# Kernel tuning notes

Measured on AMD Instinct MI355X. Metric: run time of the kernel, lower is better.

Reference implementation:

```python
import jax, jax.numpy as jnp
import numpy as np

DIM = 512
HEADS = 4
DH = 128          # dim_head
CHUNK = 16        # chunk_size
MAX_LR = 0.01     # default_adaptive_step_transform max_lr
EPS = 1e-6        # flax RMSNorm epsilon


def setup_inputs() -> dict:
    key = jax.random.key(0)
    ks = jax.random.split(key, 8)
    B, S = 2, 2048
    dim_inner = HEADS * DH
    seq = jax.random.normal(ks[0], (B, S, DIM), jnp.float32)
    store_norm_scale = jnp.ones((DIM,), jnp.float32)               # RMSNorm scale
    W_kv = (jax.random.normal(ks[1], (DIM, 2 * dim_inner)) * 0.02).astype(jnp.float32)
    W_step = (jax.random.normal(ks[2], (DIM, HEADS)) * 0.02).astype(jnp.float32)
    W_mom = (jax.random.normal(ks[3], (DIM, HEADS)) * 0.02).astype(jnp.float32)
    W_decay = (jax.random.normal(ks[4], (DIM, HEADS)) * 0.02).astype(jnp.float32)
    # past memory-MLP weights, shared init expanded to (b, h, dh, dh)
    w0 = jnp.broadcast_to((jax.random.normal(ks[5], (DH, DH)) * 0.02).astype(jnp.float32), (B, HEADS, DH, DH)) + 0.0
    w1 = jnp.broadcast_to((jax.random.normal(ks[6], (DH, DH)) * 0.02).astype(jnp.float32), (B, HEADS, DH, DH)) + 0.0
    return {"seq": seq, "store_norm_scale": store_norm_scale, "W_kv": W_kv,
            "W_step": W_step, "W_mom": W_mom, "W_decay": W_decay, "w0": w0, "w1": w1}


def _mlp(w0, w1, x):
    # MemoryMLP depth=2: x @ w0 ; silu ; @ w1
    return jax.nn.silu(x @ w0) @ w1


def _chunk_loss(w0, w1, k, lr, v):
    pred = _mlp(w0, w1, k)                       # [c, d]
    return jnp.sum(jnp.mean((pred - v) ** 2, axis=-1) * lr)


def _binop(e1, e2):
    a1, b1 = e1
    a2, b2 = e2
    return a1 * a2, a2 * b1 + b2


def _lin_scan(a, b):
    # first-order linear recurrence y_t = a_t * y_{t-1} + b_t along chunk axis (axis=2)
    return jax.lax.associative_scan(_binop, (a, b), axis=2)[1]


def _store(seq, store_norm_scale, W_kv, W_step, W_mom, W_decay, w0, w1):
    B, S, _ = seq.shape
    n = S // CHUNK
    # pre RMSNorm (with scale)
    x = seq * jax.lax.rsqrt(jnp.mean(seq * seq, axis=-1, keepdims=True) + EPS) * store_norm_scale
    # adaptive per-token lr:  sigmoid(x @ W_step) * max_lr  -> [b, h, s]
    lr = jax.nn.sigmoid(jnp.einsum('bsd,dh->bhs', x, W_step)) * MAX_LR
    # per-chunk mean -> momentum / decay factors  [b, h, n, 1]
    mean = x.reshape(B, n, CHUNK, DIM).mean(axis=2)
    mom = jax.nn.sigmoid(jnp.einsum('bnd,dh->bhn', mean, W_mom))[..., None]
    dec = jax.nn.sigmoid(jnp.einsum('bnd,dh->bhn', mean, W_decay))[..., None]
    # keys / values  [b*h, n, c, dh]
    kv = x @ W_kv
    k, v = jnp.split(kv, 2, axis=-1)
    k = k.reshape(B, n, CHUNK, HEADS, DH).transpose(0, 3, 1, 2, 4).reshape(B * HEADS, n, CHUNK, DH)
    v = v.reshape(B, n, CHUNK, HEADS, DH).transpose(0, 3, 1, 2, 4).reshape(B * HEADS, n, CHUNK, DH)
    lr_ch = lr.reshape(B, HEADS, n, CHUNK).reshape(B * HEADS, n, CHUNK)
    w0bh = w0.reshape(B * HEADS, DH, DH)
    w1bh = w1.reshape(B * HEADS, DH, DH)
    # per-chunk gradients of the MLP loss at the *past* weights (all chunks independent)
    gfn = jax.grad(_chunk_loss, argnums=(0, 1))
    gfn = jax.vmap(gfn, in_axes=(None, None, 0, 0, 0))   # over chunks n
    gfn = jax.vmap(gfn, in_axes=(0, 0, 0, 0, 0))         # over b*h
    g0, g1 = gfn(w0bh, w1bh, k, lr_ch, v)                # [b*h, n, dh, dh]
    s0 = (-g0).reshape(B, HEADS, n, DH * DH)             # surprises
    s1 = (-g1).reshape(B, HEADS, n, DH * DH)
    # momentum scan then decay scan (Titans update rule)
    m0 = _lin_scan(jnp.broadcast_to(mom, s0.shape), s0)
    m1 = _lin_scan(jnp.broadcast_to(mom, s1.shape), s1)
    u0 = _lin_scan(jnp.broadcast_to(1.0 - dec, m0.shape), m0)
    u1 = _lin_scan(jnp.broadcast_to(1.0 - dec, m1.shape), m1)
    updates = jnp.stack([u0.reshape(B, HEADS, n, DH, DH),
                         u1.reshape(B, HEADS, n, DH, DH)], axis=0)  # [2, b, h, n, dh, dh]
    return updates


def reference(seq, store_norm_scale, W_kv, W_step, W_mom, W_decay, w0, w1):
    return _store(seq, store_norm_scale, W_kv, W_step, W_mom, W_decay, w0, w1)
```

## Files before the change

kernel.cpp:

```cpp
#include <hip/hip_runtime.h>

#define DIMX 512
#define HEADSX 4
#define DHX 128
#define CHX 16
#define NCX 128
#define SX 2048
#define BX 2
#define BHX 8
#define PADF 136

typedef unsigned short ushort_t;
typedef unsigned int uint_t;
typedef short bf16x8 __attribute__((ext_vector_type(8)));
typedef float f32x4 __attribute__((ext_vector_type(4)));

__device__ __forceinline__ float sigmoidf_(float z){ return 1.0f/(1.0f + __expf(-z)); }

__device__ __forceinline__ ushort_t f2bf(float f){
  uint_t u = __float_as_uint(f);
  return (ushort_t)((u + 0x7FFFu + ((u >> 16) & 1u)) >> 16);
}
__device__ __forceinline__ uint_t pk2(float a, float b){
  return (uint_t)f2bf(a) | ((uint_t)f2bf(b) << 16);
}

__global__ __launch_bounds__(256) void k_prep(const float* __restrict__ Wkv,
    const float* __restrict__ w0, const float* __restrict__ w1,
    const float* __restrict__ scale,
    const float* __restrict__ Wstep, const float* __restrict__ Wmom,
    const float* __restrict__ Wdec,
    ushort_t* __restrict__ WkvT, ushort_t* __restrict__ w0T,
    ushort_t* __restrict__ w1T, ushort_t* __restrict__ w1n,
    float* __restrict__ wfsS, float* __restrict__ wfsM, float* __restrict__ wfsD){
  int blk = blockIdx.x; int tid = threadIdx.x;
  if (blk < 64){
    int h = blk >> 4, kt = blk & 15;
    __shared__ ushort_t tile[256][33];
    for (int i=tid; i<8192; i+=256){
      int kk = i >> 8, col = i & 255;
      int d = kt*32 + kk;
      int wcol = (col < 128) ? (h*128 + col) : (384 + h*128 + col);
      float v = scale[d] * Wkv[(size_t)d*1024 + wcol];
      tile[col][kk] = f2bf(v);
    }
    __syncthreads();
    for (int i=tid; i<8192; i+=256){
      int col = i >> 5, kk = i & 31;
      WkvT[(((size_t)h*16 + kt)*256 + col)*32 + kk] = tile[col][kk];
    }
  } else if (blk < 72){
    int bh = blk - 64;
    size_t base = (size_t)bh*16384;
    for (int i=tid; i<16384; i+=256){
      int r = i >> 7, c = i & 127;
      w0T[base + i] = f2bf(w0[base + (size_t)c*128 + r]);
      w1T[base + i] = f2bf(w1[base + (size_t)c*128 + r]);
      w1n[base + i] = f2bf(w1[base + i]);
    }
  } else {
    for (int i=tid; i<2048; i+=256){
      int d = i & 511, h = i >> 9;
      float sc = scale[d];
      wfsS[i] = sc * Wstep[d*4 + h];
      wfsM[i] = sc * Wmom [d*4 + h];
      wfsD[i] = sc * Wdec [d*4 + h];
    }
  }
}

__global__ __launch_bounds__(256) void k_fused3(const float* __restrict__ seq,
    const float* __restrict__ wfsS, const float* __restrict__ wfsM,
    const float* __restrict__ wfsD,
    const ushort_t* __restrict__ WkvT, const ushort_t* __restrict__ w0T,
    const ushort_t* __restrict__ w1T, const ushort_t* __restrict__ w1n,
    ushort_t* __restrict__ fac0, ushort_t* __restrict__ fac1,
    float* __restrict__ momw, float* __restrict__ decw){
  int blk = blockIdx.x;
  int bh = blk & 7, tq = blk >> 3;
  int b = bh >> 2, h = bh & 3;
  int tid = threadIdx.x;
  int wv = tid >> 6, lane = tid & 63;
  int t = tq*4 + wv;
  int bt = bh*NCX + t;
  int quad = lane >> 4, nl = lane & 15;
  const f32x4 zero = {0.f,0.f,0.f,0.f};

  __shared__ __align__(16) ushort_t ks_[4][16*PADF];
  __shared__ __align__(16) ushort_t as_[4][16*PADF];
  __shared__ __align__(16) ushort_t dp_[4][16*PADF];
  __shared__ __align__(16) ushort_t dh_[4][16*PADF];
  __shared__ float lr_s[4][16];
  ushort_t* ksw = ks_[wv]; ushort_t* asw = as_[wv];
  ushort_t* dpw = dp_[wv]; ushort_t* dhw = dh_[wv];

  const float* sq = seq + ((size_t)(b*SX + t*CHX) + nl)*DIMX + quad*8;
  const float* wS = wfsS + h*512 + quad*8;
  const float* wM = wfsM + h*512 + quad*8;
  const float* wD = wfsD + h*512 + quad*8;

  float ss=0.f, lp=0.f, pm=0.f, pd=0.f;
  #pragma unroll
  for (int kt=0; kt<16; kt++){
    float4 q0 = *(const float4*)(sq + kt*32);
    float4 q1 = *(const float4*)(sq + kt*32 + 4);
    float4 s0 = *(const float4*)(wS + kt*32);
    float4 s1 = *(const float4*)(wS + kt*32 + 4);
    float4 m0 = *(const float4*)(wM + kt*32);
    float4 m1 = *(const float4*)(wM + kt*32 + 4);
    float4 d0 = *(const float4*)(wD + kt*32);
    float4 d1 = *(const float4*)(wD + kt*32 + 4);
    ss += q0.x*q0.x + q0.y*q0.y + q0.z*q0.z + q0.w*q0.w
        + q1.x*q1.x + q1.y*q1.y + q1.z*q1.z + q1.w*q1.w;
    lp += q0.x*s0.x + q0.y*s0.y + q0.z*s0.z + q0.w*s0.w
        + q1.x*s1.x + q1.y*s1.y + q1.z*s1.z + q1.w*s1.w;
    pm += q0.x*m0.x + q0.y*m0.y + q0.z*m0.z + q0.w*m0.w
        + q1.x*m1.x + q1.y*m1.y + q1.z*m1.z + q1.w*m1.w;
    pd += q0.x*d0.x + q0.y*d0.y + q0.z*d0.z + q0.w*d0.w
        + q1.x*d1.x + q1.y*d1.y + q1.z*d1.z + q1.w*d1.w;
  }
  #pragma unroll
  for (int mk=16; mk<64; mk<<=1){
    ss += __shfl_xor(ss, mk, 64); lp += __shfl_xor(lp, mk, 64);
    pm += __shfl_xor(pm, mk, 64); pd += __shfl_xor(pd, mk, 64);
  }
  float rs = 1.0f / sqrtf(ss*(1.0f/DIMX) + 1e-6f);
  float lr = 0.01f * sigmoidf_(rs*lp);
  float pmr = rs*pm, pdr = rs*pd;
  #pragma unroll
  for (int mk=1; mk<16; mk<<=1){
    pmr += __shfl_xor(pmr, mk, 64); pdr += __shfl_xor(pdr, mk, 64);
  }
  if (lane==0){
    momw[bt] = sigmoidf_(pmr*(1.0f/CHX));
    decw[bt] = 1.0f - sigmoidf_(pdr*(1.0f/CHX));
  }
  if (quad==0) lr_s[wv][nl] = lr;

  union BF { bf16x8 v; uint_t u[4]; };
  f32x4 kacc[8], vacc[8];
  #pragma unroll
  for (int s=0;s<8;s++){ kacc[s]=zero; vacc[s]=zero; }
  const ushort_t* wkvh = WkvT + (size_t)h*16*256*32;
  for (int kt=0; kt<16; kt++){
    float4 q0 = *(const float4*)(sq + kt*32);
    float4 q1 = *(const float4*)(sq + kt*32 + 4);
    BF af;
    af.u[0] = pk2(q0.x*rs, q0.y*rs);
    af.u[1] = pk2(q0.z*rs, q0.w*rs);
    af.u[2] = pk2(q1.x*rs, q1.y*rs);
    af.u[3] = pk2(q1.z*rs, q1.w*rs);
    const ushort_t* wb = wkvh + ((size_t)kt*256 + nl)*32 + quad*8;
    #pragma unroll
    for (int s=0; s<8; s++){
      bf16x8 Bk = *(const bf16x8*)(wb + (size_t)(s*16)*32);
      kacc[s] = __builtin_amdgcn_mfma_f32_16x16x32_bf16(af.v, Bk, kacc[s], 0,0,0);
      bf16x8 Bv = *(const bf16x8*)(wb + (size_t)(128 + s*16)*32);
      vacc[s] = __builtin_amdgcn_mfma_f32_16x16x32_bf16(af.v, Bv, vacc[s], 0,0,0);
    }
  }
  #pragma unroll
  for (int s=0;s<8;s++){
    #pragma unroll
    for (int r=0;r<4;r++)
      ksw[(quad*4+r)*PADF + s*16 + nl] = f2bf(kacc[s][r]);
  }

  const ushort_t* w0b = w0T + (size_t)bh*16384;
  f32x4 hacc[8];
  #pragma unroll
  for (int s=0;s<8;s++) hacc[s]=zero;
  for (int kt=0; kt<4; kt++){
    bf16x8 Af = *(const bf16x8*)&ksw[nl*PADF + kt*32 + quad*8];
    #pragma unroll
    for (int s=0; s<8; s++){
      bf16x8 Bf = *(const bf16x8*)&w0b[(size_t)(s*16+nl)*128 + kt*32 + quad*8];
      hacc[s] = __builtin_amdgcn_mfma_f32_16x16x32_bf16(Af, Bf, hacc[s], 0,0,0);
    }
  }
  float sp[8][4];
  #pragma unroll
  for (int s=0;s<8;s++){
    #pragma unroll
    for (int r=0;r<4;r++){
      float hh = hacc[s][r];
      float sg = sigmoidf_(hh);
      float a  = hh*sg;
      sp[s][r] = sg*(1.0f + hh*(1.0f-sg));
      asw[(quad*4+r)*PADF + s*16 + nl] = f2bf(a);
    }
  }

  const ushort_t* w1tb = w1T + (size_t)bh*16384;
  f32x4 pacc[8];
  #pragma unroll
  for (int s=0;s<8;s++) pacc[s]=zero;
  for (int kt=0; kt<4; kt++){
    bf16x8 Af = *(const bf16x8*)&asw[nl*PADF + kt*32 + quad*8];
    #pragma unroll
    for (int s=0; s<8; s++){
      bf16x8 Bf = *(const bf16x8*)&w1tb[(size_t)(s*16+nl)*128 + kt*32 + quad*8];
      pacc[s] = __builtin_amdgcn_mfma_f32_16x16x32_bf16(Af, Bf, pacc[s], 0,0,0);
    }
  }
  float lrv[4];
  #pragma unroll
  for (int r=0;r<4;r++) lrv[r] = lr_s[wv][quad*4 + r];
  #pragma unroll
  for (int s=0;s<8;s++){
    #pragma unroll
    for (int r=0;r<4;r++){
      float dp = (2.0f/DHX)*lrv[r]*(pacc[s][r] - vacc[s][r]);
      dpw[(quad*4+r)*PADF + s*16 + nl] = f2bf(dp);
    }
  }

  const ushort_t* w1nb = w1n + (size_t)bh*16384;
  f32x4 dacc[8];
  #pragma unroll
  for (int s=0;s<8;s++) dacc[s]=zero;
  for (int kt=0; kt<4; kt++){
    bf16x8 Af = *(const bf16x8*)&dpw[nl*PADF + kt*32 + quad*8];
    #pragma unroll
    for (int s=0; s<8; s++){
      bf16x8 Bf = *(const bf16x8*)&w1nb[(size_t)(s*16+nl)*128 + kt*32 + quad*8];
      dacc[s] = __builtin_amdgcn_mfma_f32_16x16x32_bf16(Af, Bf, dacc[s], 0,0,0);
    }
  }
  #pragma unroll
  for (int s=0;s<8;s++){
    #pragma unroll
    for (int r=0;r<4;r++)
      dhw[(quad*4+r)*PADF + s*16 + nl] = f2bf(dacc[s][r]*sp[s][r]);
  }

  #pragma unroll
  for (int j=0;j<2;j++){
    int p = lane + j*64;
    ushort_t rowv[32];
    #pragma unroll
    for (int c=0;c<16;c++){ rowv[c] = ksw[c*PADF + p]; rowv[16+c] = asw[c*PADF + p]; }
    {
      ushort_t* dst = fac0 + ((size_t)bt*128 + p)*32;
      const uint4* rv = (const uint4*)rowv;
      uint4* dq = (uint4*)dst;
      dq[0]=rv[0]; dq[1]=rv[1]; dq[2]=rv[2]; dq[3]=rv[3];
    }
    #pragma unroll
    for (int c=0;c<16;c++){ rowv[c] = dhw[c*PADF + p]; rowv[16+c] = dpw[c*PADF + p]; }
    {
      ushort_t* dst = fac1 + ((size_t)bt*128 + p)*32;
      const uint4* rv = (const uint4*)rowv;
      uint4* dq = (uint4*)dst;
      dq[0]=rv[0]; dq[1]=rv[1]; dq[2]=rv[2]; dq[3]=rv[3];
    }
  }
}

__global__ __launch_bounds__(64) void k_scan3(const ushort_t* __restrict__ fac0,
    const ushort_t* __restrict__ fac1,
    const float* __restrict__ momw, const float* __restrict__ decw,
    float* __restrict__ out){
  int blk = blockIdx.x;
  int bh  = blk & 7;
  int jb  = (blk >> 3) & 7;
  int ig  = (blk >> 6) & 7;
  int mat = blk >> 9;
  int lane = threadIdx.x;
  int quad = lane >> 4, rrow = lane & 15;
  const f32x4 zero = {0.f,0.f,0.f,0.f};
  const bf16x8 fz = {0,0,0,0,0,0,0,0};

  size_t rowbase = (size_t)bh*NCX*128;
  const ushort_t* pa = fac0 + (rowbase + (size_t)(ig*16 + rrow))*32 + mat*16 + quad*8;
  const ushort_t* pb = fac1 + (rowbase + (size_t)(jb*16 + rrow))*32 + mat*16 + quad*8;
  bool act = (quad < 2);

  bf16x8 fa0=fz, fb0=fz, fa1=fz, fb1=fz;
  if (act){
    fa0 = *(const bf16x8*)(pa);
    fb0 = *(const bf16x8*)(pb);
    fa1 = *(const bf16x8*)(pa + 4096);
    fb1 = *(const bf16x8*)(pb + 4096);
  }

  f32x4 m_ = zero, u_ = zero;
  size_t obase = ((size_t)(mat*BHX + bh)*NCX)*((size_t)DHX*DHX)
               + (size_t)(ig*16 + quad*4)*DHX + (size_t)(jb*16 + rrow);
  const float* mop = momw + bh*NCX;
  const float* dep = decw + bh*NCX;

  for (int t=0; t<NCX; t+=2){
    bf16x8 na0=fz, nb0=fz, na1=fz, nb1=fz;
    if (act && (t+2 < NCX)){
      na0 = *(const bf16x8*)(pa + (size_t)(t+2)*4096);
      nb0 = *(const bf16x8*)(pb + (size_t)(t+2)*4096);
      na1 = *(const bf16x8*)(pa + (size_t)(t+3)*4096);
      nb1 = *(const bf16x8*)(pb + (size_t)(t+3)*4096);
    }
    float mo = mop[t], de = dep[t];
    f32x4 g = __builtin_amdgcn_mfma_f32_16x16x32_bf16(fa0, fb0, zero, 0,0,0);
    float* ob = out + obase + (size_t)t*(DHX*DHX);
    #pragma unroll
    for (int r=0;r<4;r++){
      m_[r] = mo*m_[r] - g[r];
      u_[r] = de*u_[r] + m_[r];
      ob[(size_t)r*DHX] = u_[r];
    }
    mo = mop[t+1]; de = dep[t+1];
    g = __builtin_amdgcn_mfma_f32_16x16x32_bf16(fa1, fb1, zero, 0,0,0);
    ob += (size_t)DHX*DHX;
    #pragma unroll
    for (int r=0;r<4;r++){
      m_[r] = mo*m_[r] - g[r];
      u_[r] = de*u_[r] + m_[r];
      ob[(size_t)r*DHX] = u_[r];
    }
    fa0=na0; fb0=nb0; fa1=na1; fb1=nb1;
  }
}

extern "C" void kernel_launch(void* const* d_in, const int* in_sizes, int n_in,
                              void* d_out, int out_size, void* d_ws, size_t ws_size,
                              hipStream_t stream) {
  (void)in_sizes; (void)n_in; (void)out_size; (void)ws_size;
  const float* seq   = (const float*)d_in[0];
  const float* scale = (const float*)d_in[1];
  const float* Wkv   = (const float*)d_in[2];
  const float* Wstep = (const float*)d_in[3];
  const float* Wmom  = (const float*)d_in[4];
  const float* Wdec  = (const float*)d_in[5];
  const float* w0    = (const float*)d_in[6];
  const float* w1    = (const float*)d_in[7];
  float* out = (float*)d_out;

  ushort_t* fac0 = (ushort_t*)d_ws;
  ushort_t* fac1 = fac0 + 4194304;
  ushort_t* WkvT = fac1 + 4194304;
  ushort_t* w0T  = WkvT + 524288;
  ushort_t* w1T  = w0T + 131072;
  ushort_t* w1n  = w1T + 131072;
  float*    momw = (float*)(w1n + 131072);
  float*    decw = momw + 1024;
  float*    wfsS = decw + 1024;
  float*    wfsM = wfsS + 2048;
  float*    wfsD = wfsM + 2048;

  k_prep<<<dim3(73), dim3(256), 0, stream>>>(Wkv, w0, w1, scale, Wstep, Wmom, Wdec,
      WkvT, w0T, w1T, w1n, wfsS, wfsM, wfsD);
  k_fused3<<<dim3(256), dim3(256), 0, stream>>>(seq, wfsS, wfsM, wfsD,
      WkvT, w0T, w1T, w1n, fac0, fac1, momw, decw);
  k_scan3<<<dim3(1024), dim3(64), 0, stream>>>(fac0, fac1, momw, decw, out);
}
```

Before: 244.0 us.

## Split fused kernel into stats, KV GEMM and per-chunk MLP kernels

Replaces the single fused kernel with three stages. A stats kernel computes the RMSNorm, lr, momentum and decay per token once and writes a bf16 normalized input. A KV GEMM kernel computes keys and values once for all heads. A per-chunk MLP-gradient kernel then runs with more blocks and the MLP output columns spread across waves. The old fused kernel re-read seq four times per head and held large accumulator arrays per wave, which limited occupancy. The new layout adds global round-trips for xhat, k and v (v kept in fp32) plus two extra launches.

```diff
diff --git a/kernel.cpp b/kernel.cpp
--- a/kernel.cpp
+++ b/kernel.cpp
@@ -25,30 +25,36 @@
   return (uint_t)f2bf(a) | ((uint_t)f2bf(b) << 16);
 }
 
-__global__ __launch_bounds__(256) void k_prep(const float* __restrict__ Wkv,
+__global__ __launch_bounds__(256) void k_prep2(const float* __restrict__ Wkv,
     const float* __restrict__ w0, const float* __restrict__ w1,
     const float* __restrict__ scale,
     const float* __restrict__ Wstep, const float* __restrict__ Wmom,
     const float* __restrict__ Wdec,
-    ushort_t* __restrict__ WkvT, ushort_t* __restrict__ w0T,
+    ushort_t* __restrict__ WkvT2, ushort_t* __restrict__ w0T,
     ushort_t* __restrict__ w1T, ushort_t* __restrict__ w1n,
     float* __restrict__ wfsS, float* __restrict__ wfsM, float* __restrict__ wfsD){
   int blk = blockIdx.x; int tid = threadIdx.x;
   if (blk < 64){
-    int h = blk >> 4, kt = blk & 15;
-    __shared__ ushort_t tile[256][33];
-    for (int i=tid; i<8192; i+=256){
-      int kk = i >> 8, col = i & 255;
-      int d = kt*32 + kk;
-      int wcol = (col < 128) ? (h*128 + col) : (384 + h*128 + col);
-      float v = scale[d] * Wkv[(size_t)d*1024 + wcol];
-      tile[col][kk] = f2bf(v);
+    int n0 = blk*16;
+    __shared__ ushort_t tile[16][520];
+    #pragma unroll
+    for (int rr=0; rr<2; rr++){
+      int k = tid*2 + rr;
+      float sc = scale[k];
+      #pragma unroll
+      for (int f=0; f<4; f++){
+        float4 v = *(const float4*)&Wkv[(size_t)k*1024 + n0 + f*4];
+        tile[f*4+0][k] = f2bf(sc*v.x);
+        tile[f*4+1][k] = f2bf(sc*v.y);
+        tile[f*4+2][k] = f2bf(sc*v.z);
+        tile[f*4+3][k] = f2bf(sc*v.w);
+      }
     }
     __syncthreads();
-    for (int i=tid; i<8192; i+=256){
-      int col = i >> 5, kk = i & 31;
-      WkvT[(((size_t)h*16 + kt)*256 + col)*32 + kk] = tile[col][kk];
-    }
+    int nr = tid >> 4, seg = tid & 15;
+    const uint4* s = (const uint4*)&tile[nr][seg*32];
+    uint4* d = (uint4*)&WkvT2[(size_t)(n0+nr)*512 + seg*32];
+    d[0]=s[0]; d[1]=s[1]; d[2]=s[2]; d[3]=s[3];
   } else if (blk < 72){
     int bh = blk - 64;
     size_t base = (size_t)bh*16384;
@@ -60,198 +66,248 @@
     }
   } else {
     for (int i=tid; i<2048; i+=256){
-      int d = i & 511, h = i >> 9;
-      float sc = scale[d];
-      wfsS[i] = sc * Wstep[d*4 + h];
-      wfsM[i] = sc * Wmom [d*4 + h];
-      wfsD[i] = sc * Wdec [d*4 + h];
-    }
-  }
-}
-
-__global__ __launch_bounds__(256) void k_fused3(const float* __restrict__ seq,
+      float sc = scale[i>>2];
+      wfsS[i] = sc * Wstep[i];
+      wfsM[i] = sc * Wmom [i];
+      wfsD[i] = sc * Wdec [i];
+    }
+  }
+}
+
+__global__ __launch_bounds__(256) void k_stats2(const float* __restrict__ seq,
     const float* __restrict__ wfsS, const float* __restrict__ wfsM,
     const float* __restrict__ wfsD,
-    const ushort_t* __restrict__ WkvT, const ushort_t* __restrict__ w0T,
-    const ushort_t* __restrict__ w1T, const ushort_t* __restrict__ w1n,
-    ushort_t* __restrict__ fac0, ushort_t* __restrict__ fac1,
+    ushort_t* __restrict__ xhat, float* __restrict__ lrbuf,
     float* __restrict__ momw, float* __restrict__ decw){
   int blk = blockIdx.x;
-  int bh = blk & 7, tq = blk >> 3;
-  int b = bh >> 2, h = bh & 3;
+  int b = blk >> 7, nc = blk & 127;
   int tid = threadIdx.x;
   int wv = tid >> 6, lane = tid & 63;
-  int t = tq*4 + wv;
-  int bt = bh*NCX + t;
+  int c = tid >> 4, sl = tid & 15;
+  size_t tok = (size_t)(b*SX + nc*CHX + c);
+  const float4* sr = (const float4*)(seq + tok*DIMX);
+  float4 q[8];
+  #pragma unroll
+  for (int jj=0; jj<8; jj++) q[jj] = sr[sl + 16*jj];
+
+  float ss=0.f;
+  float lp[4]={0,0,0,0}, pm[4]={0,0,0,0}, pd[4]={0,0,0,0};
+  #pragma unroll
+  for (int jj=0; jj<8; jj++){
+    int d0 = (sl + 16*jj)*4;
+    float qx=q[jj].x, qy=q[jj].y, qz=q[jj].z, qw=q[jj].w;
+    ss += qx*qx + qy*qy + qz*qz + qw*qw;
+    #pragma unroll
+    for (int e=0; e<4; e++){
+      float qe = (e==0)?qx:(e==1)?qy:(e==2)?qz:qw;
+      float4 tS = *(const float4*)&wfsS[(size_t)(d0+e)*4];
+      float4 tM = *(const float4*)&wfsM[(size_t)(d0+e)*4];
+      float4 tD = *(const float4*)&wfsD[(size_t)(d0+e)*4];
+      lp[0]+=qe*tS.x; lp[1]+=qe*tS.y; lp[2]+=qe*tS.z; lp[3]+=qe*tS.w;
+      pm[0]+=qe*tM.x; pm[1]+=qe*tM.y; pm[2]+=qe*tM.z; pm[3]+=qe*tM.w;
+      pd[0]+=qe*tD.x; pd[1]+=qe*tD.y; pd[2]+=qe*tD.z; pd[3]+=qe*tD.w;
+    }
+  }
+  #pragma unroll
+  for (int mk=1; mk<16; mk<<=1){
+    ss += __shfl_xor(ss, mk, 64);
+    #pragma unroll
+    for (int hh=0; hh<4; hh++){
+      lp[hh]+=__shfl_xor(lp[hh],mk,64);
+      pm[hh]+=__shfl_xor(pm[hh],mk,64);
+      pd[hh]+=__shfl_xor(pd[hh],mk,64);
+    }
+  }
+  float rs = 1.0f / sqrtf(ss*(1.0f/DIMX) + 1e-6f);
+
+  #pragma unroll
+  for (int jj=0; jj<8; jj++){
+    uint2 u;
+    u.x = pk2(q[jj].x*rs, q[jj].y*rs);
+    u.y = pk2(q[jj].z*rs, q[jj].w*rs);
+    *(uint2*)&xhat[tok*DIMX + (size_t)(sl+16*jj)*4] = u;
+  }
+  if (sl == 0){
+    #pragma unroll
+    for (int hh=0; hh<4; hh++)
+      lrbuf[(size_t)(b*HEADSX+hh)*SX + nc*CHX + c] = 0.01f * sigmoidf_(rs*lp[hh]);
+  }
+  float pmr[4], pdr[4];
+  #pragma unroll
+  for (int hh=0; hh<4; hh++){ pmr[hh]=rs*pm[hh]; pdr[hh]=rs*pd[hh]; }
+  #pragma unroll
+  for (int mk=16; mk<64; mk<<=1){
+    #pragma unroll
+    for (int hh=0; hh<4; hh++){
+      pmr[hh]+=__shfl_xor(pmr[hh],mk,64);
+      pdr[hh]+=__shfl_xor(pdr[hh],mk,64);
+    }
+  }
+  __shared__ float redm[4][4], redd[4][4];
+  if (lane == 0){
+    #pragma unroll
+    for (int hh=0; hh<4; hh++){ redm[wv][hh]=pmr[hh]; redd[wv][hh]=pdr[hh]; }
+  }
+  __syncthreads();
+  if (tid < 8){
+    int hh = tid & 3; bool isd = tid >= 4;
+    float v = isd ? (redd[0][hh]+redd[1][hh]+redd[2][hh]+redd[3][hh])
+                  : (redm[0][hh]+redm[1][hh]+redm[2][hh]+redm[3][hh]);
+    float sg = sigmoidf_(v*(1.0f/CHX));
+    int bt = (b*HEADSX+hh)*NCX + nc;
+    if (isd) decw[bt] = 1.0f - sg; else momw[bt] = sg;
+  }
+}
+
+__global__ __launch_bounds__(512) void k_kv2(const ushort_t* __restrict__ xhat,
+    const ushort_t* __restrict__ WkvT2,
+    ushort_t* __restrict__ kbuf, float* __restrict__ vbuf){
+  int blk = blockIdx.x;
+  int nb = blk >> 6, mb = blk & 63;
+  int b = mb >> 5;
+  int mrow0 = (mb & 31) * 64;
+  int isv = nb >> 2, h = nb & 3;
+  int bh = b*HEADSX + h;
+  int tid = threadIdx.x;
+  int wv = tid >> 6, lane = tid & 63;
   int quad = lane >> 4, nl = lane & 15;
   const f32x4 zero = {0.f,0.f,0.f,0.f};
 
-  __shared__ __align__(16) ushort_t ks_[4][16*PADF];
-  __shared__ __align__(16) ushort_t as_[4][16*PADF];
-  __shared__ __align__(16) ushort_t dp_[4][16*PADF];
-  __shared__ __align__(16) ushort_t dh_[4][16*PADF];
-  __shared__ float lr_s[4][16];
-  ushort_t* ksw = ks_[wv]; ushort_t* asw = as_[wv];
-  ushort_t* dpw = dp_[wv]; ushort_t* dhw = dh_[wv];
-
-  const float* sq = seq + ((size_t)(b*SX + t*CHX) + nl)*DIMX + quad*8;
-  const float* wS = wfsS + h*512 + quad*8;
-  const float* wM = wfsM + h*512 + quad*8;
-  const float* wD = wfsD + h*512 + quad*8;
-
-  float ss=0.f, lp=0.f, pm=0.f, pd=0.f;
+  const ushort_t* xb = xhat + ((size_t)b*SX + mrow0)*DIMX + nl*DIMX + quad*8;
+  const ushort_t* brow = WkvT2 + ((size_t)nb*128 + wv*16 + nl)*DIMX + quad*8;
+
+  f32x4 acc[4] = {zero,zero,zero,zero};
   #pragma unroll
   for (int kt=0; kt<16; kt++){
-    float4 q0 = *(const float4*)(sq + kt*32);
-    float4 q1 = *(const float4*)(sq + kt*32 + 4);
-    float4 s0 = *(const float4*)(wS + kt*32);
-    float4 s1 = *(const float4*)(wS + kt*32 + 4);
-    float4 m0 = *(const float4*)(wM + kt*32);
-    float4 m1 = *(const float4*)(wM + kt*32 + 4);
-    float4 d0 = *(const float4*)(wD + kt*32);
-    float4 d1 = *(const float4*)(wD + kt*32 + 4);
-    ss += q0.x*q0.x + q0.y*q0.y + q0.z*q0.z + q0.w*q0.w
-        + q1.x*q1.x + q1.y*q1.y + q1.z*q1.z + q1.w*q1.w;
-    lp += q0.x*s0.x + q0.y*s0.y + q0.z*s0.z + q0.w*s0.w
-        + q1.x*s1.x + q1.y*s1.y + q1.z*s1.z + q1.w*s1.w;
-    pm += q0.x*m0.x + q0.y*m0.y + q0.z*m0.z + q0.w*m0.w
-        + q1.x*m1.x + q1.y*m1.y + q1.z*m1.z + q1.w*m1.w;
-    pd += q0.x*d0.x + q0.y*d0.y + q0.z*d0.z + q0.w*d0.w
-        + q1.x*d1.x + q1.y*d1.y + q1.z*d1.z + q1.w*d1.w;
-  }
-  #pragma unroll
-  for (int mk=16; mk<64; mk<<=1){
-    ss += __shfl_xor(ss, mk, 64); lp += __shfl_xor(lp, mk, 64);
-    pm += __shfl_xor(pm, mk, 64); pd += __shfl_xor(pd, mk, 64);
-  }
-  float rs = 1.0f / sqrtf(ss*(1.0f/DIMX) + 1e-6f);
-  float lr = 0.01f * sigmoidf_(rs*lp);
-  float pmr = rs*pm, pdr = rs*pd;
-  #pragma unroll
-  for (int mk=1; mk<16; mk<<=1){
-    pmr += __shfl_xor(pmr, mk, 64); pdr += __shfl_xor(pdr, mk, 64);
-  }
-  if (lane==0){
-    momw[bt] = sigmoidf_(pmr*(1.0f/CHX));
-    decw[bt] = 1.0f - sigmoidf_(pdr*(1.0f/CHX));
-  }
-  if (quad==0) lr_s[wv][nl] = lr;
-
-  union BF { bf16x8 v; uint_t u[4]; };
-  f32x4 kacc[8], vacc[8];
-  #pragma unroll
-  for (int s=0;s<8;s++){ kacc[s]=zero; vacc[s]=zero; }
-  const ushort_t* wkvh = WkvT + (size_t)h*16*256*32;
-  for (int kt=0; kt<16; kt++){
-    float4 q0 = *(const float4*)(sq + kt*32);
-    float4 q1 = *(const float4*)(sq + kt*32 + 4);
-    BF af;
-    af.u[0] = pk2(q0.x*rs, q0.y*rs);
-    af.u[1] = pk2(q0.z*rs, q0.w*rs);
-    af.u[2] = pk2(q1.x*rs, q1.y*rs);
-    af.u[3] = pk2(q1.z*rs, q1.w*rs);
-    const ushort_t* wb = wkvh + ((size_t)kt*256 + nl)*32 + quad*8;
-    #pragma unroll
-    for (int s=0; s<8; s++){
-      bf16x8 Bk = *(const bf16x8*)(wb + (size_t)(s*16)*32);
-      kacc[s] = __builtin_amdgcn_mfma_f32_16x16x32_bf16(af.v, Bk, kacc[s], 0,0,0);
-      bf16x8 Bv = *(const bf16x8*)(wb + (size_t)(128 + s*16)*32);
-      vacc[s] = __builtin_amdgcn_mfma_f32_16x16x32_bf16(af.v, Bv, vacc[s], 0,0,0);
-    }
-  }
-  #pragma unroll
-  for (int s=0;s<8;s++){
-    #pragma unroll
-    for (int r=0;r<4;r++)
-      ksw[(quad*4+r)*PADF + s*16 + nl] = f2bf(kacc[s][r]);
-  }
+    bf16x8 Bf = *(const bf16x8*)(brow + kt*32);
+    #pragma unroll
+    for (int mf=0; mf<4; mf++){
+      bf16x8 Af = *(const bf16x8*)(xb + (size_t)(mf*16)*DIMX + kt*32);
+      acc[mf] = __builtin_amdgcn_mfma_f32_16x16x32_bf16(Af, Bf, acc[mf], 0,0,0);
+    }
+  }
+  int p = wv*16 + nl;
+  #pragma unroll
+  for (int mf=0; mf<4; mf++){
+    int t = (mb & 31)*4 + mf;
+    size_t bt = (size_t)bh*NCX + t;
+    if (isv){
+      #pragma unroll
+      for (int r=0;r<4;r++)
+        vbuf[(bt*16 + quad*4 + r)*128 + p] = acc[mf][r];
+    } else {
+      #pragma unroll
+      for (int r=0;r<4;r++)
+        kbuf[(bt*16 + quad*4 + r)*128 + p] = f2bf(acc[mf][r]);
+    }
+  }
+}
+
+__global__ __launch_bounds__(128) void k_mlp2(const ushort_t* __restrict__ kbuf,
+    const float* __restrict__ vbuf, const float* __restrict__ lrbuf,
+    const ushort_t* __restrict__ w0T, const ushort_t* __restrict__ w1T,
+    const ushort_t* __restrict__ w1n,
+    ushort_t* __restrict__ fac0, ushort_t* __restrict__ fac1){
+  int blk = blockIdx.x;
+  int bh = blk & 7, t = blk >> 3;
+  size_t bt = (size_t)bh*NCX + t;
+  int tid = threadIdx.x;
+  int wv = tid >> 6, lane = tid & 63;
+  int quad = lane >> 4, nl = lane & 15;
+  const f32x4 zero = {0.f,0.f,0.f,0.f};
+  __shared__ __align__(16) ushort_t as_[16*PADF];
+  __shared__ __align__(16) ushort_t dp_[16*PADF];
+  __shared__ __align__(16) ushort_t dh_[16*PADF];
+
+  const ushort_t* kb = kbuf + bt*16*128;
 
   const ushort_t* w0b = w0T + (size_t)bh*16384;
-  f32x4 hacc[8];
-  #pragma unroll
-  for (int s=0;s<8;s++) hacc[s]=zero;
+  f32x4 hacc[4] = {zero,zero,zero,zero};
+  #pragma unroll
   for (int kt=0; kt<4; kt++){
-    bf16x8 Af = *(const bf16x8*)&ksw[nl*PADF + kt*32 + quad*8];
-    #pragma unroll
-    for (int s=0; s<8; s++){
-      bf16x8 Bf = *(const bf16x8*)&w0b[(size_t)(s*16+nl)*128 + kt*32 + quad*8];
-      hacc[s] = __builtin_amdgcn_mfma_f32_16x16x32_bf16(Af, Bf, hacc[s], 0,0,0);
-    }
-  }
-  float sp[8][4];
-  #pragma unroll
-  for (int s=0;s<8;s++){
-    #pragma unroll
-    for (int r=0;r<4;r++){
-      float hh = hacc[s][r];
+    bf16x8 Af = *(const bf16x8*)(kb + (size_t)nl*128 + kt*32 + quad*8);
+    #pragma unroll
+    for (int j=0; j<4; j++){
+      int n = (wv*4+j)*16 + nl;
+      bf16x8 Bf = *(const bf16x8*)(w0b + (size_t)n*128 + kt*32 + quad*8);
+      hacc[j] = __builtin_amdgcn_mfma_f32_16x16x32_bf16(Af, Bf, hacc[j], 0,0,0);
+    }
+  }
+  float sp[4][4];
+  #pragma unroll
+  for (int j=0; j<4; j++){
+    #pragma unroll
+    for (int r=0; r<4; r++){
+      float hh = hacc[j][r];
       float sg = sigmoidf_(hh);
-      float a  = hh*sg;
-      sp[s][r] = sg*(1.0f + hh*(1.0f-sg));
-      asw[(quad*4+r)*PADF + s*16 + nl] = f2bf(a);
-    }
-  }
+      sp[j][r] = sg*(1.0f + hh*(1.0f-sg));
+      as_[(quad*4+r)*PADF + (wv*4+j)*16 + nl] = f2bf(hh*sg);
+    }
+  }
+  __syncthreads();
 
   const ushort_t* w1tb = w1T + (size_t)bh*16384;
-  f32x4 pacc[8];
-  #pragma unroll
-  for (int s=0;s<8;s++) pacc[s]=zero;
+  f32x4 pacc[4] = {zero,zero,zero,zero};
+  #pragma unroll
   for (int kt=0; kt<4; kt++){
-    bf16x8 Af = *(const bf16x8*)&asw[nl*PADF + kt*32 + quad*8];
-    #pragma unroll
-    for (int s=0; s<8; s++){
-      bf16x8 Bf = *(const bf16x8*)&w1tb[(size_t)(s*16+nl)*128 + kt*32 + quad*8];
-      pacc[s] = __builtin_amdgcn_mfma_f32_16x16x32_bf16(Af, Bf, pacc[s], 0,0,0);
+    bf16x8 Af = *(const bf16x8*)&as_[nl*PADF + kt*32 + quad*8];
+    #pragma unroll
+    for (int j=0; j<4; j++){
+      int n = (wv*4+j)*16 + nl;
+      bf16x8 Bf = *(const bf16x8*)(w1tb + (size_t)n*128 + kt*32 + quad*8);
+      pacc[j] = __builtin_amdgcn_mfma_f32_16x16x32_bf16(Af, Bf, pacc[j], 0,0,0);
     }
   }
   float lrv[4];
   #pragma unroll
-  for (int r=0;r<4;r++) lrv[r] = lr_s[wv][quad*4 + r];
-  #pragma unroll
-  for (int s=0;s<8;s++){
-    #pragma unroll
-    for (int r=0;r<4;r++){
-      float dp = (2.0f/DHX)*lrv[r]*(pacc[s][r] - vacc[s][r]);
-      dpw[(quad*4+r)*PADF + s*16 + nl] = f2bf(dp);
-    }
-  }
+  for (int r=0; r<4; r++) lrv[r] = lrbuf[(size_t)bh*SX + t*CHX + quad*4 + r];
+  #pragma unroll
+  for (int j=0; j<4; j++){
+    #pragma unroll
+    for (int r=0; r<4; r++){
+      int c = quad*4 + r;
+      float vv = vbuf[(bt*16 + c)*128 + (wv*4+j)*16 + nl];
+      float dp = (2.0f/DHX)*lrv[r]*(pacc[j][r] - vv);
+      dp_[c*PADF + (wv*4+j)*16 + nl] = f2bf(dp);
+    }
+  }
+  __syncthreads();
 
   const ushort_t* w1nb = w1n + (size_t)bh*16384;
-  f32x4 dacc[8];
-  #pragma unroll
-  for (int s=0;s<8;s++) dacc[s]=zero;
+  f32x4 dacc[4] = {zero,zero,zero,zero};
+  #pragma unroll
   for (int kt=0; kt<4; kt++){
-    bf16x8 Af = *(const bf16x8*)&dpw[nl*PADF + kt*32 + quad*8];
-    #pragma unroll
-    for (int s=0; s<8; s++){
-      bf16x8 Bf = *(const bf16x8*)&w1nb[(size_t)(s*16+nl)*128 + kt*32 + quad*8];
-      dacc[s] = __builtin_amdgcn_mfma_f32_16x16x32_bf16(Af, Bf, dacc[s], 0,0,0);
-    }
-  }
-  #pragma unroll
-  for (int s=0;s<8;s++){
-    #pragma unroll
-    for (int r=0;r<4;r++)
-      dhw[(quad*4+r)*PADF + s*16 + nl] = f2bf(dacc[s][r]*sp[s][r]);
-  }
-
-  #pragma unroll
-  for (int j=0;j<2;j++){
-    int p = lane + j*64;
+    bf16x8 Af = *(const bf16x8*)&dp_[nl*PADF + kt*32 + quad*8];
+    #pragma unroll
+    for (int j=0; j<4; j++){
+      int n = (wv*4+j)*16 + nl;
+      bf16x8 Bf = *(const bf16x8*)(w1nb + (size_t)n*128 + kt*32 + quad*8);
+      dacc[j] = __builtin_amdgcn_mfma_f32_16x16x32_bf16(Af, Bf, dacc[j], 0,0,0);
+    }
+  }
+  #pragma unroll
+  for (int j=0; j<4; j++){
+    #pragma unroll
+    for (int r=0; r<4; r++)
+      dh_[(quad*4+r)*PADF + (wv*4+j)*16 + nl] = f2bf(dacc[j][r]*sp[j][r]);
+  }
+  __syncthreads();
+
+  {
+    int p = tid;
     ushort_t rowv[32];
     #pragma unroll
-    for (int c=0;c<16;c++){ rowv[c] = ksw[c*PADF + p]; rowv[16+c] = asw[c*PADF + p]; }
+    for (int c=0; c<16; c++){ rowv[c] = kb[(size_t)c*128 + p]; rowv[16+c] = as_[c*PADF + p]; }
     {
-      ushort_t* dst = fac0 + ((size_t)bt*128 + p)*32;
+      uint4* dq = (uint4*)(fac0 + (bt*128 + p)*32);
       const uint4* rv = (const uint4*)rowv;
-      uint4* dq = (uint4*)dst;
       dq[0]=rv[0]; dq[1]=rv[1]; dq[2]=rv[2]; dq[3]=rv[3];
     }
     #pragma unroll
-    for (int c=0;c<16;c++){ rowv[c] = dhw[c*PADF + p]; rowv[16+c] = dpw[c*PADF + p]; }
+    for (int c=0; c<16; c++){ rowv[c] = dh_[c*PADF + p]; rowv[16+c] = dp_[c*PADF + p]; }
     {
-      ushort_t* dst = fac1 + ((size_t)bt*128 + p)*32;
+      uint4* dq = (uint4*)(fac1 + (bt*128 + p)*32);
       const uint4* rv = (const uint4*)rowv;
-      uint4* dq = (uint4*)dst;
       dq[0]=rv[0]; dq[1]=rv[1]; dq[2]=rv[2]; dq[3]=rv[3];
     }
   }
@@ -333,22 +389,30 @@
   const float* w0    = (const float*)d_in[6];
   const float* w1    = (const float*)d_in[7];
   float* out = (float*)d_out;
-
-  ushort_t* fac0 = (ushort_t*)d_ws;
-  ushort_t* fac1 = fac0 + 4194304;
-  ushort_t* WkvT = fac1 + 4194304;
-  ushort_t* w0T  = WkvT + 524288;
-  ushort_t* w1T  = w0T + 131072;
-  ushort_t* w1n  = w1T + 131072;
-  float*    momw = (float*)(w1n + 131072);
-  float*    decw = momw + 1024;
-  float*    wfsS = decw + 1024;
-  float*    wfsM = wfsS + 2048;
-  float*    wfsD = wfsM + 2048;
-
-  k_prep<<<dim3(73), dim3(256), 0, stream>>>(Wkv, w0, w1, scale, Wstep, Wmom, Wdec,
-      WkvT, w0T, w1T, w1n, wfsS, wfsM, wfsD);
-  k_fused3<<<dim3(256), dim3(256), 0, stream>>>(seq, wfsS, wfsM, wfsD,
-      WkvT, w0T, w1T, w1n, fac0, fac1, momw, decw);
+  float* ws  = (float*)d_ws;
+
+  ushort_t* fac0  = (ushort_t*)(ws);
+  ushort_t* fac1  = (ushort_t*)(ws + 2097152);
+  ushort_t* WkvT2 = (ushort_t*)(ws + 4194304);
+  ushort_t* w0T   = (ushort_t*)(ws + 4456448);
+  ushort_t* w1T   = (ushort_t*)(ws + 4521984);
+  ushort_t* w1n   = (ushort_t*)(ws + 4587520);
+  ushort_t* xhat  = (ushort_t*)(ws + 4653056);
+  ushort_t* kbuf  = (ushort_t*)(ws + 5701632);
+  float*    vbuf  = ws + 6750208;
+  float*    lrbuf = ws + 8847360;
+  float*    momw  = ws + 8863744;
+  float*    decw  = ws + 8864768;
+  float*    wfsS  = ws + 8865792;
+  float*    wfsM  = ws + 8867840;
+  float*    wfsD  = ws + 8869888;
+
+  k_prep2<<<dim3(73), dim3(256), 0, stream>>>(Wkv, w0, w1, scale, Wstep, Wmom, Wdec,
+      WkvT2, w0T, w1T, w1n, wfsS, wfsM, wfsD);
+  k_stats2<<<dim3(BX*NCX), dim3(256), 0, stream>>>(seq, wfsS, wfsM, wfsD,
+      xhat, lrbuf, momw, decw);
+  k_kv2<<<dim3(512), dim3(512), 0, stream>>>(xhat, WkvT2, kbuf, vbuf);
+  k_mlp2<<<dim3(BHX*NCX), dim3(128), 0, stream>>>(kbuf, vbuf, lrbuf,
+      w0T, w1T, w1n, fac0, fac1);
   k_scan3<<<dim3(1024), dim3(64), 0, stream>>>(fac0, fac1, momw, decw, out);
 }
```

Result: slower. 260.8 us (+6.9%).
